# Optimization experiments

Measured on AMD Instinct MI355X. Metric: run time of the kernel, lower is better.

## Reference

```python
import jax, jax.numpy as jnp
import numpy as np

D_MODEL = 1024
N_HEADS = 16
N_KV = 4
HEAD_DIM = D_MODEL // N_HEADS  # 64
SEQ = 2048
BATCH = 2
CAP = 50.0
EPS = 1e-5
THETA = 10000.0


def setup_inputs() -> dict:
    key = jax.random.key(0)
    ks = jax.random.split(key, 5)
    s = 0.02  # keep pre-attention logits in a sane range
    return {
        'x':   jax.random.normal(ks[0], (BATCH, SEQ, D_MODEL), dtype=jnp.float32),
        'w_q': jax.random.normal(ks[1], (D_MODEL, N_HEADS * HEAD_DIM), dtype=jnp.float32) * s,
        'w_k': jax.random.normal(ks[2], (D_MODEL, N_KV * HEAD_DIM), dtype=jnp.float32) * s,
        'w_v': jax.random.normal(ks[3], (D_MODEL, N_KV * HEAD_DIM), dtype=jnp.float32) * s,
        'w_o': jax.random.normal(ks[4], (N_HEADS * HEAD_DIM, D_MODEL), dtype=jnp.float32) * s,
    }


def _rms_norm(x, eps=EPS):
    return x * jax.lax.rsqrt(jnp.mean(jnp.square(x), axis=-1, keepdims=True) + eps)


def _rope_cos_sin(seq_len, head_dim, theta=THETA):
    inv_freq = 1.0 / (theta ** (jnp.arange(0, head_dim, 2, dtype=jnp.float32) / head_dim))
    freqs = jnp.arange(seq_len, dtype=jnp.float32)[:, None] * inv_freq[None, :]  # (S, d/2)
    return jnp.cos(freqs)[None, :, None, :], jnp.sin(freqs)[None, :, None, :]  # (1,S,1,d/2)


def _apply_rope(x, cos, sin):
    d = x.shape[-1] // 2
    x1, x2 = x[..., :d], x[..., d:]
    return jnp.concatenate([x1 * cos - x2 * sin, x2 * cos + x1 * sin], axis=-1).astype(x.dtype)


def reference(x, w_q, w_k, w_v, w_o):
    B, S, _ = x.shape
    q = (x @ w_q).reshape(B, S, N_HEADS, HEAD_DIM)
    k = (x @ w_k).reshape(B, S, N_KV, HEAD_DIM)
    v = (x @ w_v).reshape(B, S, N_KV, HEAD_DIM)

    # QK RMS-norm (no learned scale)
    q = _rms_norm(q)
    k = _rms_norm(k)

    cos, sin = _rope_cos_sin(S, HEAD_DIM)
    q = _apply_rope(q, cos, sin)
    k = _apply_rope(k, cos, sin)

    # GQA: repeat kv heads to match query heads
    rep = N_HEADS // N_KV
    k = jnp.repeat(k, rep, axis=2)
    v = jnp.repeat(v, rep, axis=2)

    scores = jnp.einsum('bqhd,bkhd->bhqk', q, k) / np.sqrt(HEAD_DIM).astype(np.float32)
    # softcap in float32, as in the original
    scores = jnp.tanh(scores.astype(jnp.float32) / CAP) * CAP
    causal = jnp.tril(jnp.ones((S, S), dtype=bool))  # (S, S)
    scores = jnp.where(causal[None, None], scores, -jnp.inf)
    probs = jax.nn.softmax(scores, axis=-1)  # dropout=0.0 -> identity

    y = jnp.einsum('bhqk,bkhd->bqhd', probs, v).reshape(B, S, N_HEADS * HEAD_DIM)
    return y @ w_o
```

## Files before the change

### kernel.cpp

```cpp
#include <hip/hip_runtime.h>
#include <hip/hip_bf16.h>
#include <math.h>

#define D_MODEL 1024
#define N_HEADS 16
#define N_KV 4
#define HEAD_DIM 64
#define SEQ 2048
#define BATCH 2
#define M_TOK (BATCH * SEQ)

typedef unsigned int u32;
typedef unsigned short u16;
typedef __attribute__((ext_vector_type(8))) short short8;
typedef __attribute__((ext_vector_type(4))) float f32x4;
typedef __attribute__((ext_vector_type(16))) float f32x16;
typedef __attribute__((ext_vector_type(2))) float f32x2;

#define AS1 __attribute__((address_space(1)))
#define AS3 __attribute__((address_space(3)))

__device__ __forceinline__ u16 f2bf(float f) {
  union { __hip_bfloat16 h; u16 u; } c; c.h = __float2bfloat16(f); return c.u;
}
__device__ __forceinline__ u32 cvtpk(float lo, float hi) {
  u32 r; asm("v_cvt_pk_bf16_f32 %0, %1, %2" : "=v"(r) : "v"(lo), "v"(hi)); return r;
}
__device__ __forceinline__ void plswap(u32& a, u32& b) {
  asm volatile("v_permlane32_swap_b32 %0, %1" : "+v"(a), "+v"(b));
}
__device__ __forceinline__ float exp2fast(float x) { return __builtin_amdgcn_exp2f(x); }
__device__ __forceinline__ float rcpfast(float x) { return __builtin_amdgcn_rcpf(x); }
__device__ __forceinline__ f32x2 pk_mul(f32x2 a, f32x2 b) {
  f32x2 d; asm("v_pk_mul_f32 %0, %1, %2" : "=v"(d) : "v"(a), "v"(b)); return d;
}
__device__ __forceinline__ f32x2 pk_fma(f32x2 a, f32x2 b, f32x2 c) {
  f32x2 d; asm("v_pk_fma_f32 %0, %1, %2, %3" : "=v"(d) : "v"(a), "v"(b), "v"(c)); return d;
}

__global__ __launch_bounds__(256) void prep_kernel(const float* __restrict__ x,
                                                   const float* __restrict__ wq,
                                                   const float* __restrict__ wk,
                                                   const float* __restrict__ wv,
                                                   const float* __restrict__ wo,
                                                   u16* __restrict__ xb,
                                                   u16* __restrict__ wT,
                                                   u16* __restrict__ woT) {
  int bx = blockIdx.x;
  if (bx < 512) {
    const size_t base = (size_t)bx * 8192;
#pragma unroll
    for (int j = 0; j < 4; ++j) {
      size_t e = base + j * 2048 + threadIdx.x * 8;
      float4 f0 = *(const float4*)(x + e);
      float4 f1 = *(const float4*)(x + e + 4);
      uint4 u;
      u.x = cvtpk(f0.x, f0.y); u.y = cvtpk(f0.z, f0.w);
      u.z = cvtpk(f1.x, f1.y); u.w = cvtpk(f1.z, f1.w);
      *(uint4*)(xb + e) = u;
    }
    return;
  }
  bx -= 512;
  __shared__ float t[32][33];
  const float* src; u16* dst; int N, ntm, nts;
  if (bx < 1024)      { src = wq; dst = wT;                 N = 1024; ntm = 31; nts = 5; }
  else if (bx < 1280) { bx -= 1024; src = wk; dst = wT + (1024 << 10); N = 256; ntm = 7; nts = 3; }
  else if (bx < 1536) { bx -= 1280; src = wv; dst = wT + (1280 << 10); N = 256; ntm = 7; nts = 3; }
  else                { bx -= 1536; src = wo; dst = woT;    N = 1024; ntm = 31; nts = 5; }
  const int n0 = (bx & ntm) << 5, k0 = (bx >> nts) << 5;
  const int xx = threadIdx.x & 31, y = threadIdx.x >> 5;
#pragma unroll
  for (int i = 0; i < 4; ++i) {
    int r = y + (i << 3);
    t[r][xx] = src[(size_t)(k0 + r) * N + n0 + xx];
  }
  __syncthreads();
#pragma unroll
  for (int i = 0; i < 4; ++i) {
    int r = y + (i << 3);
    dst[(size_t)(n0 + r) * 1024 + k0 + xx] = f2bf(t[xx][r]);
  }
}

__global__ __launch_bounds__(256, 2) void qkvgemm_kernel(const u16* __restrict__ xb,
                                                         const u16* __restrict__ wT,
                                                         u16* __restrict__ Qbf,
                                                         u16* __restrict__ Kbf,
                                                         u16* __restrict__ Vt) {
  __shared__ uint4 SM[4][512];
  const int tid = threadIdx.x;
  const int w = tid >> 6, l = tid & 63;
  const int wr = w >> 1, wc = w & 1;
  int wg = ((int)blockIdx.x & 7) * 48 + ((int)blockIdx.x >> 3);
  const int mt = wg / 12, nb = wg - mt * 12;
  const int m0 = mt << 7;

  f32x4 acc[4][4];
#pragma unroll
  for (int m = 0; m < 4; ++m)
#pragma unroll
    for (int n = 0; n < 4; ++n)
#pragma unroll
      for (int j = 0; j < 4; ++j) acc[m][n][j] = 0.f;

  auto stage = [&](int buf, int k0) {
    const u16* Ab = xb + (size_t)m0 * 1024 + k0;
#pragma unroll
    for (int r = 0; r < 2; ++r) {
      int i = (w << 1) + r;
      int row = (i << 4) + (l >> 2);
      const u16* g = Ab + (size_t)row * 1024 + ((l & 3) << 3);
      __builtin_amdgcn_global_load_lds((const AS1 void*)g,
          (AS3 void*)((char*)SM + (buf << 13) + (i << 10)), 16, 0, 0);
    }
    const u16* Bb = wT + (size_t)(nb << 7) * 1024 + k0;
#pragma unroll
    for (int r = 0; r < 2; ++r) {
      int i = (w << 1) + r;
      int row = (i << 4) + (l >> 2);
      const u16* g = Bb + (size_t)row * 1024 + ((l & 3) << 3);
      __builtin_amdgcn_global_load_lds((const AS1 void*)g,
          (AS3 void*)((char*)SM + ((2 + buf) << 13) + (i << 10)), 16, 0, 0);
    }
  };

  stage(0, 0);
#pragma unroll 1
  for (int kt = 0; kt < 32; ++kt) {
    __syncthreads();
    if (kt + 1 < 32) stage((kt + 1) & 1, (kt + 1) << 5);
    const char* Ab = (const char*)SM + ((kt & 1) << 13);
    const char* Bb = (const char*)SM + ((2 + (kt & 1)) << 13);
    short8 af[4], bf[4];
#pragma unroll
    for (int m = 0; m < 4; ++m)
      af[m] = *(const short8*)(Ab + ((wr * 64 + m * 16 + (l & 15)) << 6) + ((l >> 4) << 4));
#pragma unroll
    for (int n = 0; n < 4; ++n)
      bf[n] = *(const short8*)(Bb + ((wc * 64 + n * 16 + (l & 15)) << 6) + ((l >> 4) << 4));
#pragma unroll
    for (int m = 0; m < 4; ++m)
#pragma unroll
      for (int n = 0; n < 4; ++n)
        acc[m][n] = __builtin_amdgcn_mfma_f32_16x16x32_bf16(af[m], bf[n], acc[m][n], 0, 0, 0);
  }

  __syncthreads();
  const int b = m0 >> 11;
  const int pos0 = (m0 & 2047) + wr * 64;
  const int lg = l >> 4, lc = l & 15;
  u16* lds = (u16*)((char*)SM + (w << 13));

  if (nb < 10) {
    float rs[4][4];
#pragma unroll
    for (int m = 0; m < 4; ++m)
#pragma unroll
      for (int j = 0; j < 4; ++j) {
        float ssq = 0.f;
#pragma unroll
        for (int n = 0; n < 4; ++n) ssq = fmaf(acc[m][n][j], acc[m][n][j], ssq);
        ssq += __shfl_xor(ssq, 1); ssq += __shfl_xor(ssq, 2);
        ssq += __shfl_xor(ssq, 4); ssq += __shfl_xor(ssq, 8);
        rs[m][j] = rsqrtf(ssq * (1.f / 64.f) + 1e-5f);
      }
    const float osc = (nb < 8) ? 0.0025f : 1.0f;
    const float invf0 = powf(10000.0f, (float)lc * (-1.f / 32.f));
    const float invf1 = powf(10000.0f, (float)(lc + 16) * (-1.f / 32.f));
#pragma unroll
    for (int m = 0; m < 4; ++m) {
#pragma unroll
      for (int j = 0; j < 4; ++j) {
        const int row = m * 16 + lg * 4 + j;
        const float pos = (float)(pos0 + row);
        float s0, c0, s1, c1;
        sincosf(pos * invf0, &s0, &c0);
        sincosf(pos * invf1, &s1, &c1);
        const float r_ = rs[m][j];
        float x0 = acc[m][0][j] * r_, x1 = acc[m][1][j] * r_;
        float x2 = acc[m][2][j] * r_, x3 = acc[m][3][j] * r_;
        u16 o0 = f2bf((x0 * c0 - x2 * s0) * osc);
        u16 o1 = f2bf((x1 * c1 - x3 * s1) * osc);
        u16 o2 = f2bf((x2 * c0 + x0 * s0) * osc);
        u16 o3 = f2bf((x3 * c1 + x1 * s1) * osc);
        const int rb = row << 6, xr = (row & 7) << 3;
        lds[rb + (lc ^ xr)] = o0;
        lds[rb + ((16 + lc) ^ xr)] = o1;
        lds[rb + ((32 + lc) ^ xr)] = o2;
        lds[rb + ((48 + lc) ^ xr)] = o3;
      }
    }
  } else {
#pragma unroll
    for (int m = 0; m < 4; ++m)
#pragma unroll
      for (int n = 0; n < 4; ++n) {
        const int d = n * 16 + lc;
        const int tok = m * 16 + lg * 4;
        uint2 u;
        u.x = cvtpk(acc[m][n][0], acc[m][n][1]);
        u.y = cvtpk(acc[m][n][2], acc[m][n][3]);
        *(uint2*)(lds + (d << 6) + (tok ^ ((d & 7) << 3))) = u;
      }
  }
  __syncthreads();

  u16* gp; int rstride;
  if (nb < 8)       { gp = Qbf + ((size_t)((b * 16 + nb * 2 + wc) * 2048 + pos0) << 6); rstride = 64; }
  else if (nb < 10) { gp = Kbf + ((size_t)((b * 4 + (nb - 8) * 2 + wc) * 2048 + pos0) << 6); rstride = 64; }
  else              { gp = Vt + (((size_t)((b * 4 + (nb - 10) * 2 + wc) * 64)) << 11) + pos0; rstride = 2048; }
#pragma unroll
  for (int ic = 0; ic < 8; ++ic) {
    const int c = (ic << 6) + l;
    const int row = c >> 3, col8 = (c & 7) << 3;
    uint4 v = *(const uint4*)(lds + (row << 6) + (col8 ^ ((row & 7) << 3)));
    *(uint4*)(gp + (size_t)row * rstride + col8) = v;
  }
}

__global__ __launch_bounds__(256, 2) void gemm_kernel(const u16* __restrict__ A,
                                                      const u16* __restrict__ BT,
                                                      float* __restrict__ C) {
  __shared__ uint4 SM[4][512];
  const int tid = threadIdx.x;
  const int w = tid >> 6, l = tid & 63;
  const int wr = w >> 1, wc = w & 1;
  int wg = ((int)blockIdx.x & 7) * 32 + ((int)blockIdx.x >> 3);
  const int m0 = (wg >> 3) << 7, n0 = (wg & 7) << 7;

  f32x4 acc[4][4];
#pragma unroll
  for (int m = 0; m < 4; ++m)
#pragma unroll
    for (int n = 0; n < 4; ++n)
#pragma unroll
      for (int j = 0; j < 4; ++j) acc[m][n][j] = 0.f;

  auto stage = [&](int buf, int k0) {
    const u16* Ab = A + (size_t)m0 * 1024 + k0;
#pragma unroll
    for (int r = 0; r < 2; ++r) {
      int i = (w << 1) + r;
      int row = (i << 4) + (l >> 2);
      const u16* g = Ab + (size_t)row * 1024 + ((l & 3) << 3);
      __builtin_amdgcn_global_load_lds((const AS1 void*)g,
          (AS3 void*)((char*)SM + (buf << 13) + (i << 10)), 16, 0, 0);
    }
    const u16* Bb = BT + (size_t)n0 * 1024 + k0;
#pragma unroll
    for (int r = 0; r < 2; ++r) {
      int i = (w << 1) + r;
      int row = (i << 4) + (l >> 2);
      const u16* g = Bb + (size_t)row * 1024 + ((l & 3) << 3);
      __builtin_amdgcn_global_load_lds((const AS1 void*)g,
          (AS3 void*)((char*)SM + ((2 + buf) << 13) + (i << 10)), 16, 0, 0);
    }
  };

  stage(0, 0);
#pragma unroll 1
  for (int kt = 0; kt < 32; ++kt) {
    __syncthreads();
    if (kt + 1 < 32) stage((kt + 1) & 1, (kt + 1) << 5);
    const char* Ab = (const char*)SM + ((kt & 1) << 13);
    const char* Bb = (const char*)SM + ((2 + (kt & 1)) << 13);
    short8 af[4], bf[4];
#pragma unroll
    for (int m = 0; m < 4; ++m)
      af[m] = *(const short8*)(Ab + ((wr * 64 + m * 16 + (l & 15)) << 6) + ((l >> 4) << 4));
#pragma unroll
    for (int n = 0; n < 4; ++n)
      bf[n] = *(const short8*)(Bb + ((wc * 64 + n * 16 + (l & 15)) << 6) + ((l >> 4) << 4));
#pragma unroll
    for (int m = 0; m < 4; ++m)
#pragma unroll
      for (int n = 0; n < 4; ++n)
        acc[m][n] = __builtin_amdgcn_mfma_f32_16x16x32_bf16(af[m], bf[n], acc[m][n], 0, 0, 0);
  }

#pragma unroll
  for (int m = 0; m < 4; ++m) {
    int row0 = m0 + wr * 64 + m * 16 + ((l >> 4) << 2);
#pragma unroll
    for (int n = 0; n < 4; ++n) {
      int col = n0 + wc * 64 + n * 16 + (l & 15);
#pragma unroll
      for (int j = 0; j < 4; ++j)
        C[(size_t)(row0 + j) * 1024 + col] = acc[m][n][j];
    }
  }
}

__device__ __forceinline__ short8 rdfrag(const uint4* lds, int row, int cb) {
  int byte = ((row << 7) + cb) ^ ((row & 7) << 4);
  return *(const short8*)((const char*)lds + byte);
}

__global__ __launch_bounds__(256, 2) void attn_kernel(const u16* __restrict__ Qbf,
                                                      const u16* __restrict__ Kbf,
                                                      const u16* __restrict__ Vt,
                                                      u16* __restrict__ ybf) {
  __shared__ uint4 KV[4][512];
  const int tid = threadIdx.x;
  const int g = blockIdx.x & 7;
  const int j = 63 - (blockIdx.x >> 3);
  const int b = g >> 2, hkv = g & 3;
  const int w = tid >> 6, l = tid & 63;
  const int ql = l & 31, myh = l >> 5;
  const int h = hkv * 4 + w;
  const int q0 = j << 5;
  const int qg = q0 + ql;

  const u16* Kg = Kbf + (((size_t)g) << 11) * 64;
  const u16* Vg = Vt + (((size_t)g) << 6) * 2048;

  short8 bq[4];
  {
    const u16* Qg = Qbf + ((size_t)((b * 16 + h) * 2048 + qg)) * 64 + myh * 8;
    bq[0] = *(const short8*)(Qg);
    bq[1] = *(const short8*)(Qg + 16);
    bq[2] = *(const short8*)(Qg + 32);
    bq[3] = *(const short8*)(Qg + 48);
  }

  f32x16 o0, o1;
#pragma unroll
  for (int i = 0; i < 16; ++i) { o0[i] = 0.f; o1[i] = 0.f; }
  float l_run = 0.f;

  const int KT = (j >> 1) + 1;

  auto stage = [&](int buf, int kt) {
    const u16* gk = Kg + ((size_t)(kt << 6)) * 64;
    const u16* gv = Vg + (kt << 6);
#pragma unroll
    for (int i = 0; i < 2; ++i) {
      int c = tid + (i << 8);
      int row = c >> 3, off = c & 7;
      uint4 kk4 = *(const uint4*)(gk + row * 64 + (off << 3));
      uint4 vv4 = *(const uint4*)(gv + (size_t)row * 2048 + (off << 3));
      int byte = ((row << 7) + (off << 4)) ^ ((row & 7) << 4);
      *(uint4*)((char*)KV[buf << 1] + byte) = kk4;
      *(uint4*)((char*)KV[(buf << 1) + 1] + byte) = vv4;
    }
  };

  stage(0, 0);

  const float PC2 = -0.33333333f;
  const float SC1 = 72.13475204444817f;
  const float SC0 = -11.541560327111708f;
  const f32x2 PC2v = {PC2, PC2};
  const f32x2 SC1v = {SC1, SC1};
  const f32x2 SC0v = {SC0, SC0};
  const f32x2 ONEv = {1.0f, 1.0f};

#pragma unroll 1
  for (int kt = 0; kt < KT; ++kt) {
    const int buf = kt & 1;
    __syncthreads();
    if (kt + 1 < KT) stage(buf ^ 1, kt + 1);
    const bool last = (kt == KT - 1);
    const bool havehi = !last || (j & 1);
    const uint4* Kl = KV[buf << 1];
    const uint4* Vl = KV[(buf << 1) + 1];

    f32x16 s0, s1;
#pragma unroll
    for (int i = 0; i < 16; ++i) { s0[i] = 0.f; s1[i] = 0.f; }
    __builtin_amdgcn_s_setprio(1);
#pragma unroll
    for (int c = 0; c < 4; ++c) {
      short8 ak = rdfrag(Kl, ql, (c << 5) + (myh << 4));
      s0 = __builtin_amdgcn_mfma_f32_32x32x16_bf16(ak, bq[c], s0, 0, 0, 0);
    }
    if (havehi) {
#pragma unroll
      for (int c = 0; c < 4; ++c) {
        short8 ak = rdfrag(Kl, 32 + ql, (c << 5) + (myh << 4));
        s1 = __builtin_amdgcn_mfma_f32_32x32x16_bf16(ak, bq[c], s1, 0, 0, 0);
      }
    }
    __builtin_amdgcn_s_setprio(0);

    float lsum = 0.f;
    auto cap_full = [&](f32x16& s) {
#pragma unroll
      for (int p = 0; p < 8; ++p) {
        f32x2 z; z.x = s[2 * p]; z.y = s[2 * p + 1];
        f32x2 z2 = pk_mul(z, z);
        f32x2 zc = pk_fma(z2, PC2v, ONEv);
        f32x2 zs = pk_mul(z, SC1v);
        f32x2 ar = pk_fma(zs, zc, SC0v);
        float p0 = exp2fast(ar.x);
        float p1 = exp2fast(ar.y);
        s[2 * p] = p0; s[2 * p + 1] = p1;
        lsum += p0; lsum += p1;
      }
    };
    auto cap_diag = [&](f32x16& s) {
#pragma unroll
      for (int i = 0; i < 16; ++i) {
        int kl = (i & 3) + ((i >> 2) << 3) + (myh << 2);
        float z = s[i];
        float zc = fmaf(z * z, PC2, 1.0f);
        float p = exp2fast(fmaf(z * zc, SC1, SC0));
        p = (kl <= ql) ? p : 0.f;
        s[i] = p; lsum += p;
      }
    };
    if (!last)       { cap_full(s0); cap_full(s1); }
    else if (j & 1)  { cap_full(s0); cap_diag(s1); }
    else             { cap_diag(s0); }
    l_run += lsum;

    short8 pa[4];
    auto mkpa = [&](const f32x16& P, int c0) {
#pragma unroll
      for (int ci = 0; ci < 2; ++ci) {
        const int rb = ci << 3;
        u32 A = cvtpk(P[rb + 0], P[rb + 1]);
        u32 Cw = cvtpk(P[rb + 2], P[rb + 3]);
        u32 B = cvtpk(P[rb + 4], P[rb + 5]);
        u32 D = cvtpk(P[rb + 6], P[rb + 7]);
        plswap(A, B); plswap(Cw, D);
        union { u32 u[4]; short8 s; } pw_;
        pw_.u[0] = A; pw_.u[1] = Cw; pw_.u[2] = B; pw_.u[3] = D;
        pa[c0 + ci] = pw_.s;
      }
    };
    mkpa(s0, 0);
    if (havehi) mkpa(s1, 2);

    __builtin_amdgcn_s_setprio(1);
#pragma unroll
    for (int c = 0; c < 2; ++c) {
      short8 av = rdfrag(Vl, ql, (c << 5) + (myh << 4));
      o0 = __builtin_amdgcn_mfma_f32_32x32x16_bf16(av, pa[c], o0, 0, 0, 0);
      short8 av1 = rdfrag(Vl, 32 + ql, (c << 5) + (myh << 4));
      o1 = __builtin_amdgcn_mfma_f32_32x32x16_bf16(av1, pa[c], o1, 0, 0, 0);
    }
    if (havehi) {
#pragma unroll
      for (int c = 2; c < 4; ++c) {
        short8 av = rdfrag(Vl, ql, (c << 5) + (myh << 4));
        o0 = __builtin_amdgcn_mfma_f32_32x32x16_bf16(av, pa[c], o0, 0, 0, 0);
        short8 av1 = rdfrag(Vl, 32 + ql, (c << 5) + (myh << 4));
        o1 = __builtin_amdgcn_mfma_f32_32x32x16_bf16(av1, pa[c], o1, 0, 0, 0);
      }
    }
    __builtin_amdgcn_s_setprio(0);
  }

  float lr = l_run + __shfl_xor(l_run, 32);
  float rl = rcpfast(lr);
  u16* yr = ybf + ((size_t)(b * 2048 + qg)) * 1024 + h * 64;
#pragma unroll
  for (int i = 0; i < 16; i += 2) {
    int dof = (i & 3) + ((i >> 2) << 3) + (myh << 2);
    *(u32*)(yr + dof) = cvtpk(o0[i] * rl, o0[i + 1] * rl);
    *(u32*)(yr + 32 + dof) = cvtpk(o1[i] * rl, o1[i + 1] * rl);
  }
}

extern "C" void kernel_launch(void* const* d_in, const int* in_sizes, int n_in,
                              void* d_out, int out_size, void* d_ws, size_t ws_size,
                              hipStream_t stream) {
  (void)in_sizes; (void)n_in; (void)out_size; (void)ws_size;
  const float* x  = (const float*)d_in[0];
  const float* wq = (const float*)d_in[1];
  const float* wk = (const float*)d_in[2];
  const float* wv = (const float*)d_in[3];
  const float* wo = (const float*)d_in[4];
  float* out = (float*)d_out;

  char* ws = (char*)d_ws;
  u16* xb  = (u16*)ws;
  u16* ybf = (u16*)(ws + (8u << 20));
  u16* woT = (u16*)(ws + (16u << 20));
  u16* wT  = (u16*)(ws + (18u << 20));
  u16* Qbf = (u16*)(ws + (21u << 20));
  u16* Kbf = (u16*)(ws + (29u << 20));
  u16* Vt  = (u16*)(ws + (31u << 20));

  prep_kernel<<<dim3(3072), 256, 0, stream>>>(x, wq, wk, wv, wo, xb, wT, woT);
  qkvgemm_kernel<<<dim3(384), 256, 0, stream>>>(xb, wT, Qbf, Kbf, Vt);
  attn_kernel<<<dim3(512), 256, 0, stream>>>(Qbf, Kbf, Vt, ybf);
  gemm_kernel<<<dim3(256), 256, 0, stream>>>(ybf, woT, out);
}
```

Before: 105.9 us.

## Split long causal attention rows across two blocks and merge in output GEMM

Attention query blocks in the second half of the sequence are split into two KV ranges, each written as unnormalised bf16 output plus row sums to separate buffers. The output projection GEMM loads both partials, sums them, and applies the reciprocal normaliser while staging A into LDS. This is meant to remove the causal load imbalance and the long tail of the heaviest attention blocks. In exchange it adds extra global traffic and replaces async global-to-LDS loads for A with register-staged loads and conversion work. Attention occupancy is also raised to three blocks per unit.

```diff
diff --git a/kernel.cpp b/kernel.cpp
--- a/kernel.cpp
+++ b/kernel.cpp
@@ -22,6 +22,9 @@
 
 __device__ __forceinline__ u16 f2bf(float f) {
   union { __hip_bfloat16 h; u16 u; } c; c.h = __float2bfloat16(f); return c.u;
+}
+__device__ __forceinline__ float bf2f(u16 v) {
+  union { u32 u; float f; } c; c.u = (u32)v << 16; return c.f;
 }
 __device__ __forceinline__ u32 cvtpk(float lo, float hi) {
   u32 r; asm("v_cvt_pk_bf16_f32 %0, %1, %2" : "=v"(r) : "v"(lo), "v"(hi)); return r;
@@ -219,7 +222,10 @@
   }
 }
 
-__global__ __launch_bounds__(256, 2) void gemm_kernel(const u16* __restrict__ A,
+__global__ __launch_bounds__(256, 2) void gemm_kernel(const u16* __restrict__ O0,
+                                                      const u16* __restrict__ O1,
+                                                      const float* __restrict__ L0,
+                                                      const float* __restrict__ L1,
                                                       const u16* __restrict__ BT,
                                                       float* __restrict__ C) {
   __shared__ uint4 SM[4][512];
@@ -228,6 +234,8 @@
   const int wr = w >> 1, wc = w & 1;
   int wg = ((int)blockIdx.x & 7) * 32 + ((int)blockIdx.x >> 3);
   const int m0 = (wg >> 3) << 7, n0 = (wg & 7) << 7;
+  const bool heavy = (m0 & 2047) >= 1024;
+  const int bb = m0 >> 11;
 
   f32x4 acc[4][4];
 #pragma unroll
@@ -237,16 +245,44 @@
 #pragma unroll
       for (int j = 0; j < 4; ++j) acc[m][n][j] = 0.f;
 
-  auto stage = [&](int buf, int k0) {
-    const u16* Ab = A + (size_t)m0 * 1024 + k0;
-#pragma unroll
-    for (int r = 0; r < 2; ++r) {
-      int i = (w << 1) + r;
-      int row = (i << 4) + (l >> 2);
-      const u16* g = Ab + (size_t)row * 1024 + ((l & 3) << 3);
-      __builtin_amdgcn_global_load_lds((const AS1 void*)g,
-          (AS3 void*)((char*)SM + (buf << 13) + (i << 10)), 16, 0, 0);
-    }
+  short8 ra0[2], ra1[2];
+  float rla[2];
+
+  auto ldA = [&](int k0) {
+    const int h = k0 >> 6;
+#pragma unroll
+    for (int i2 = 0; i2 < 2; ++i2) {
+      int c = tid + (i2 << 8);
+      int row = c >> 2, q = c & 3;
+      int rowg = m0 + row;
+      ra0[i2] = *(const short8*)(O0 + (size_t)rowg * 1024 + k0 + (q << 3));
+      float la = L0[rowg * 16 + h];
+      if (heavy) {
+        int hrow = rowg - (bb + 1) * 1024;
+        ra1[i2] = *(const short8*)(O1 + (size_t)hrow * 1024 + k0 + (q << 3));
+        la += L1[hrow * 16 + h];
+      }
+      rla[i2] = rcpfast(la);
+    }
+  };
+  auto stA = [&](int buf) {
+#pragma unroll
+    for (int i2 = 0; i2 < 2; ++i2) {
+      int c = tid + (i2 << 8);
+      int row = c >> 2, q = c & 3;
+      uint4 u;
+      float rl = rla[i2];
+#pragma unroll
+      for (int e = 0; e < 4; ++e) {
+        float v0 = bf2f((u16)ra0[i2][2 * e]);
+        float v1 = bf2f((u16)ra0[i2][2 * e + 1]);
+        if (heavy) { v0 += bf2f((u16)ra1[i2][2 * e]); v1 += bf2f((u16)ra1[i2][2 * e + 1]); }
+        ((u32*)&u)[e] = cvtpk(v0 * rl, v1 * rl);
+      }
+      *(uint4*)((char*)SM + (buf << 13) + (row << 6) + (q << 4)) = u;
+    }
+  };
+  auto stB = [&](int buf, int k0) {
     const u16* Bb = BT + (size_t)n0 * 1024 + k0;
 #pragma unroll
     for (int r = 0; r < 2; ++r) {
@@ -258,11 +294,12 @@
     }
   };
 
-  stage(0, 0);
+  ldA(0); stA(0); stB(0, 0);
 #pragma unroll 1
   for (int kt = 0; kt < 32; ++kt) {
     __syncthreads();
-    if (kt + 1 < 32) stage((kt + 1) & 1, (kt + 1) << 5);
+    const bool more = (kt + 1 < 32);
+    if (more) { ldA((kt + 1) << 5); stB((kt + 1) & 1, (kt + 1) << 5); }
     const char* Ab = (const char*)SM + ((kt & 1) << 13);
     const char* Bb = (const char*)SM + ((2 + (kt & 1)) << 13);
     short8 af[4], bf[4];
@@ -277,6 +314,7 @@
 #pragma unroll
       for (int n = 0; n < 4; ++n)
         acc[m][n] = __builtin_amdgcn_mfma_f32_16x16x32_bf16(af[m], bf[n], acc[m][n], 0, 0, 0);
+    if (more) stA((kt + 1) & 1);
   }
 
 #pragma unroll
@@ -297,14 +335,23 @@
   return *(const short8*)((const char*)lds + byte);
 }
 
-__global__ __launch_bounds__(256, 2) void attn_kernel(const u16* __restrict__ Qbf,
+__global__ __launch_bounds__(256, 3) void attn_kernel(const u16* __restrict__ Qbf,
                                                       const u16* __restrict__ Kbf,
                                                       const u16* __restrict__ Vt,
-                                                      u16* __restrict__ ybf) {
+                                                      u16* __restrict__ O0,
+                                                      u16* __restrict__ O1,
+                                                      float* __restrict__ L0,
+                                                      float* __restrict__ L1) {
   __shared__ uint4 KV[4][512];
   const int tid = threadIdx.x;
   const int g = blockIdx.x & 7;
-  const int j = 63 - (blockIdx.x >> 3);
+  const int u = blockIdx.x >> 3;
+  int j, kt0, kt1; bool diagEnd;
+  if (u < 32)      { j = u;       kt0 = 0;  kt1 = (j >> 1) + 1; diagEnd = true; }
+  else if (u < 64) { j = u;       kt0 = 0;  kt1 = 16;           diagEnd = false; }
+  else             { j = 127 - u; kt0 = 16; kt1 = (j >> 1) + 1; diagEnd = true; }
+  const bool slot1 = (u >= 64);
+
   const int b = g >> 2, hkv = g & 3;
   const int w = tid >> 6, l = tid & 63;
   const int ql = l & 31, myh = l >> 5;
@@ -328,8 +375,6 @@
 #pragma unroll
   for (int i = 0; i < 16; ++i) { o0[i] = 0.f; o1[i] = 0.f; }
   float l_run = 0.f;
-
-  const int KT = (j >> 1) + 1;
 
   auto stage = [&](int buf, int kt) {
     const u16* gk = Kg + ((size_t)(kt << 6)) * 64;
@@ -346,7 +391,7 @@
     }
   };
 
-  stage(0, 0);
+  stage(0, kt0);
 
   const float PC2 = -0.33333333f;
   const float SC1 = 72.13475204444817f;
@@ -357,11 +402,11 @@
   const f32x2 ONEv = {1.0f, 1.0f};
 
 #pragma unroll 1
-  for (int kt = 0; kt < KT; ++kt) {
+  for (int kt = kt0; kt < kt1; ++kt) {
     const int buf = kt & 1;
     __syncthreads();
-    if (kt + 1 < KT) stage(buf ^ 1, kt + 1);
-    const bool last = (kt == KT - 1);
+    if (kt + 1 < kt1) stage(buf ^ 1, kt + 1);
+    const bool last = diagEnd && (kt == kt1 - 1);
     const bool havehi = !last || (j & 1);
     const uint4* Kl = KV[buf << 1];
     const uint4* Vl = KV[(buf << 1) + 1];
@@ -453,15 +498,19 @@
     __builtin_amdgcn_s_setprio(0);
   }
 
-  float lr = l_run + __shfl_xor(l_run, 32);
-  float rl = rcpfast(lr);
-  u16* yr = ybf + ((size_t)(b * 2048 + qg)) * 1024 + h * 64;
+  size_t rowbase;
+  u16* Ob; float* Lb;
+  if (!slot1) { Ob = O0; Lb = L0; rowbase = (size_t)(b * 2048 + qg); }
+  else        { Ob = O1; Lb = L1; rowbase = (size_t)(b * 1024 + qg - 1024); }
+  u16* yr = Ob + rowbase * 1024 + h * 64;
 #pragma unroll
   for (int i = 0; i < 16; i += 2) {
     int dof = (i & 3) + ((i >> 2) << 3) + (myh << 2);
-    *(u32*)(yr + dof) = cvtpk(o0[i] * rl, o0[i + 1] * rl);
-    *(u32*)(yr + 32 + dof) = cvtpk(o1[i] * rl, o1[i + 1] * rl);
-  }
+    *(u32*)(yr + dof) = cvtpk(o0[i], o0[i + 1]);
+    *(u32*)(yr + 32 + dof) = cvtpk(o1[i], o1[i + 1]);
+  }
+  float lr = l_run + __shfl_xor(l_run, 32);
+  if (l < 32) Lb[rowbase * 16 + h] = lr;
 }
 
 extern "C" void kernel_launch(void* const* d_in, const int* in_sizes, int n_in,
@@ -477,15 +526,18 @@
 
   char* ws = (char*)d_ws;
   u16* xb  = (u16*)ws;
-  u16* ybf = (u16*)(ws + (8u << 20));
+  u16* O0  = (u16*)(ws + (8u << 20));
   u16* woT = (u16*)(ws + (16u << 20));
   u16* wT  = (u16*)(ws + (18u << 20));
   u16* Qbf = (u16*)(ws + (21u << 20));
   u16* Kbf = (u16*)(ws + (29u << 20));
   u16* Vt  = (u16*)(ws + (31u << 20));
+  u16* O1  = (u16*)(ws + (33u << 20));
+  float* L0 = (float*)(ws + (37u << 20));
+  float* L1 = (float*)(ws + (37u << 20) + (256u << 10));
 
   prep_kernel<<<dim3(3072), 256, 0, stream>>>(x, wq, wk, wv, wo, xb, wT, woT);
   qkvgemm_kernel<<<dim3(384), 256, 0, stream>>>(xb, wT, Qbf, Kbf, Vt);
-  attn_kernel<<<dim3(512), 256, 0, stream>>>(Qbf, Kbf, Vt, ybf);
-  gemm_kernel<<<dim3(256), 256, 0, stream>>>(ybf, woT, out);
-}
+  attn_kernel<<<dim3(768), 256, 0, stream>>>(Qbf, Kbf, Vt, O0, O1, L0, L1);
+  gemm_kernel<<<dim3(256), 256, 0, stream>>>(O0, O1, L0, L1, woT, out);
+}
```

Result: slower. 111.4 us (+5.1%).

## Split long causal attention rows across two blocks and merge partials

Applied to the files above, without the earlier changes.

Query tiles in the second half of each sequence are split along the key dimension into two blocks, which raises the grid from 512 to 768 blocks and evens out per-block work. Each half writes unnormalized bf16 partial outputs plus row sums to workspace, and a new combine kernel adds them, normalizes, and writes the attention output. Launch bounds also move to 3 blocks per CU. The costs are an extra kernel launch, extra global traffic for the partials, and bf16 rounding of the partials before they are summed. Merging without a max rescale is only valid because the softcap bounds the logits.

```diff
diff --git a/kernel.cpp b/kernel.cpp
--- a/kernel.cpp
+++ b/kernel.cpp
@@ -22,6 +22,9 @@
 
 __device__ __forceinline__ u16 f2bf(float f) {
   union { __hip_bfloat16 h; u16 u; } c; c.h = __float2bfloat16(f); return c.u;
+}
+__device__ __forceinline__ float bf2f(u16 v) {
+  union { u32 u; float f; } c; c.u = (u32)v << 16; return c.f;
 }
 __device__ __forceinline__ u32 cvtpk(float lo, float hi) {
   u32 r; asm("v_cvt_pk_bf16_f32 %0, %1, %2" : "=v"(r) : "v"(lo), "v"(hi)); return r;
@@ -292,19 +295,53 @@
   }
 }
 
+__global__ __launch_bounds__(256) void combine_kernel(const u16* __restrict__ P0,
+                                                      const u16* __restrict__ P1,
+                                                      const float* __restrict__ L0,
+                                                      const float* __restrict__ L1,
+                                                      u16* __restrict__ ybf) {
+  const int hrow = (blockIdx.x << 1) + (threadIdx.x >> 7);
+  const int chunk = threadIdx.x & 127;
+  const int h = chunk >> 3;
+  const int b = hrow >> 10, posl = hrow & 1023;
+  const size_t tok = (size_t)(b * 2048 + 1024 + posl);
+  const float rl = rcpfast(L0[hrow * 16 + h] + L1[hrow * 16 + h]);
+  uint4 a = *(const uint4*)(P0 + ((size_t)hrow << 10) + (chunk << 3));
+  uint4 c = *(const uint4*)(P1 + ((size_t)hrow << 10) + (chunk << 3));
+  uint4 o;
+#pragma unroll
+  for (int e = 0; e < 4; ++e) {
+    u32 ua = ((const u32*)&a)[e], uc = ((const u32*)&c)[e];
+    float v0 = (bf2f((u16)(ua & 0xffff)) + bf2f((u16)(uc & 0xffff))) * rl;
+    float v1 = (bf2f((u16)(ua >> 16)) + bf2f((u16)(uc >> 16))) * rl;
+    ((u32*)&o)[e] = cvtpk(v0, v1);
+  }
+  *(uint4*)(ybf + tok * 1024 + (chunk << 3)) = o;
+}
+
 __device__ __forceinline__ short8 rdfrag(const uint4* lds, int row, int cb) {
   int byte = ((row << 7) + cb) ^ ((row & 7) << 4);
   return *(const short8*)((const char*)lds + byte);
 }
 
-__global__ __launch_bounds__(256, 2) void attn_kernel(const u16* __restrict__ Qbf,
+__global__ __launch_bounds__(256, 3) void attn_kernel(const u16* __restrict__ Qbf,
                                                       const u16* __restrict__ Kbf,
                                                       const u16* __restrict__ Vt,
-                                                      u16* __restrict__ ybf) {
+                                                      u16* __restrict__ ybf,
+                                                      u16* __restrict__ P0,
+                                                      u16* __restrict__ P1,
+                                                      float* __restrict__ L0,
+                                                      float* __restrict__ L1) {
   __shared__ uint4 KV[4][512];
   const int tid = threadIdx.x;
   const int g = blockIdx.x & 7;
-  const int j = 63 - (blockIdx.x >> 3);
+  const int u = blockIdx.x >> 3;
+  int j, kt0, kt1; bool diagEnd;
+  if (u < 32)      { j = u;       kt0 = 0;  kt1 = (j >> 1) + 1; diagEnd = true; }
+  else if (u < 64) { j = u;       kt0 = 0;  kt1 = 16;           diagEnd = false; }
+  else             { j = 127 - u; kt0 = 16; kt1 = (j >> 1) + 1; diagEnd = true; }
+  const bool slot1 = (u >= 64);
+
   const int b = g >> 2, hkv = g & 3;
   const int w = tid >> 6, l = tid & 63;
   const int ql = l & 31, myh = l >> 5;
@@ -328,8 +365,6 @@
 #pragma unroll
   for (int i = 0; i < 16; ++i) { o0[i] = 0.f; o1[i] = 0.f; }
   float l_run = 0.f;
-
-  const int KT = (j >> 1) + 1;
 
   auto stage = [&](int buf, int kt) {
     const u16* gk = Kg + ((size_t)(kt << 6)) * 64;
@@ -346,7 +381,7 @@
     }
   };
 
-  stage(0, 0);
+  stage(0, kt0);
 
   const float PC2 = -0.33333333f;
   const float SC1 = 72.13475204444817f;
@@ -357,11 +392,11 @@
   const f32x2 ONEv = {1.0f, 1.0f};
 
 #pragma unroll 1
-  for (int kt = 0; kt < KT; ++kt) {
+  for (int kt = kt0; kt < kt1; ++kt) {
     const int buf = kt & 1;
     __syncthreads();
-    if (kt + 1 < KT) stage(buf ^ 1, kt + 1);
-    const bool last = (kt == KT - 1);
+    if (kt + 1 < kt1) stage(buf ^ 1, kt + 1);
+    const bool last = diagEnd && (kt == kt1 - 1);
     const bool havehi = !last || (j & 1);
     const uint4* Kl = KV[buf << 1];
     const uint4* Vl = KV[(buf << 1) + 1];
@@ -454,13 +489,27 @@
   }
 
   float lr = l_run + __shfl_xor(l_run, 32);
-  float rl = rcpfast(lr);
-  u16* yr = ybf + ((size_t)(b * 2048 + qg)) * 1024 + h * 64;
-#pragma unroll
-  for (int i = 0; i < 16; i += 2) {
-    int dof = (i & 3) + ((i >> 2) << 3) + (myh << 2);
-    *(u32*)(yr + dof) = cvtpk(o0[i] * rl, o0[i + 1] * rl);
-    *(u32*)(yr + 32 + dof) = cvtpk(o1[i] * rl, o1[i + 1] * rl);
+  if (u < 32) {
+    float rl = rcpfast(lr);
+    u16* yr = ybf + ((size_t)(b * 2048 + qg)) * 1024 + h * 64;
+#pragma unroll
+    for (int i = 0; i < 16; i += 2) {
+      int dof = (i & 3) + ((i >> 2) << 3) + (myh << 2);
+      *(u32*)(yr + dof) = cvtpk(o0[i] * rl, o0[i + 1] * rl);
+      *(u32*)(yr + 32 + dof) = cvtpk(o1[i] * rl, o1[i + 1] * rl);
+    }
+  } else {
+    const size_t hrow = (size_t)(b * 1024 + qg - 1024);
+    u16* Ob = slot1 ? P1 : P0;
+    float* Lb = slot1 ? L1 : L0;
+    u16* yr = Ob + (hrow << 10) + h * 64;
+#pragma unroll
+    for (int i = 0; i < 16; i += 2) {
+      int dof = (i & 3) + ((i >> 2) << 3) + (myh << 2);
+      *(u32*)(yr + dof) = cvtpk(o0[i], o0[i + 1]);
+      *(u32*)(yr + 32 + dof) = cvtpk(o1[i], o1[i + 1]);
+    }
+    if (l < 32) Lb[hrow * 16 + h] = lr;
   }
 }
 
@@ -483,9 +532,14 @@
   u16* Qbf = (u16*)(ws + (21u << 20));
   u16* Kbf = (u16*)(ws + (29u << 20));
   u16* Vt  = (u16*)(ws + (31u << 20));
+  u16* P0  = (u16*)(ws + (33u << 20));
+  u16* P1  = (u16*)(ws + (37u << 20));
+  float* L0 = (float*)(ws + (41u << 20));
+  float* L1 = (float*)(ws + (41u << 20) + (128u << 10));
 
   prep_kernel<<<dim3(3072), 256, 0, stream>>>(x, wq, wk, wv, wo, xb, wT, woT);
   qkvgemm_kernel<<<dim3(384), 256, 0, stream>>>(xb, wT, Qbf, Kbf, Vt);
-  attn_kernel<<<dim3(512), 256, 0, stream>>>(Qbf, Kbf, Vt, ybf);
+  attn_kernel<<<dim3(768), 256, 0, stream>>>(Qbf, Kbf, Vt, ybf, P0, P1, L0, L1);
+  combine_kernel<<<dim3(1024), 256, 0, stream>>>(P0, P1, L0, L1, ybf);
   gemm_kernel<<<dim3(256), 256, 0, stream>>>(ybf, woT, out);
 }
```

Measured after the change: 94.66 us, median of 3. 10.6% less time.
